# Kernel tuning notes

Measured on AMD Instinct MI355X. Metric: run time of the kernel, lower is better.

The kernel has to match this reference:

```python
import jax, jax.numpy as jnp
import numpy as np

N = 8  # block_size

def _dct_matrix(n):
    m = np.zeros((n, n), dtype=np.float32)
    for k in range(n):
        for t in range(n):
            if k == 0:
                m[k, t] = np.sqrt(1.0 / n)
            else:
                m[k, t] = np.sqrt(2.0 / n) * np.cos(np.pi * k * (2 * t + 1) / (2 * n))
    return m

def _zigzag(n):
    idxs = np.zeros((n, n), dtype=np.int64)
    idx = 0
    for s in range(2 * n - 1):
        if s % 2 == 0:
            rng = range(min(s, n - 1), max(0, s - n + 1) - 1, -1)
        else:
            rng = range(max(0, s - n + 1), min(s, n - 1) + 1)
        for i in rng:
            j = s - i
            if 0 <= i < n and 0 <= j < n:
                idxs[i, j] = idx
                idx += 1
    return idxs

def _band_masks(n):
    zz = _zigzag(n)
    total = n * n
    lo_t, hi_t = total // 3, 2 * total // 3
    low = (zz < lo_t).astype(np.float32)
    mid = ((zz >= lo_t) & (zz < hi_t)).astype(np.float32)
    high = (zz >= hi_t).astype(np.float32)
    return low, mid, high

_D = jnp.asarray(_dct_matrix(N))
_LOW, _MID, _HIGH = (jnp.asarray(m) for m in _band_masks(N))

def setup_inputs() -> dict:
    key = jax.random.key(0)
    x = jax.random.normal(key, (16, 3, 512, 512), dtype=jnp.float32)
    band_scale = jnp.ones((3,), dtype=jnp.float32)
    return {"x": x, "band_scale": band_scale}

def reference(x, band_scale):
    B, C, H, W = x.shape
    pad_h = (N - H % N) % N
    pad_w = (N - W % N) % N
    if pad_h > 0 or pad_w > 0:
        x = jnp.pad(x, ((0, 0), (0, 0), (0, pad_h), (0, pad_w)), mode="reflect")
    Hp, Wp = x.shape[2], x.shape[3]
    nH, nW = Hp // N, Wp // N
    # [B,C,nH,N,nW,N] -> blocks [B,C,nH,nW,N,N]
    blocks = x.reshape(B, C, nH, N, nW, N).transpose(0, 1, 2, 4, 3, 5)
    # 2D DCT-II: D @ X @ D^T
    coeffs = jnp.einsum("km,bchwmn,ln->bchwkl", _D, blocks, _D)

    def idct_band(mask, scale):
        c = coeffs * mask
        # IDCT: D^T @ C @ D
        sp = jnp.einsum("km,bchwkl,ln->bchwmn", _D, c, _D)
        out = sp.transpose(0, 1, 2, 4, 3, 5).reshape(B, C, Hp, Wp)
        return out[:, :, :H, :W] * scale

    low = idct_band(_LOW, band_scale[0])
    mid = idct_band(_MID, band_scale[1])
    high = idct_band(_HIGH, band_scale[2])
    return (low, mid, high)
```

## Files before the change

### kernel.cpp

```cpp
#include <hip/hip_runtime.h>

#define IMG   512
#define NIMG  48
#define PLANE (IMG * IMG)
#define OUTCH ((size_t)NIMG * PLANE)
#define NTHREADS (NIMG * 64 * 64)

__device__ constexpr float Dm[8][8] = {
  { 0.3535533905932738f, 0.3535533905932738f, 0.3535533905932738f, 0.3535533905932738f,
    0.3535533905932738f, 0.3535533905932738f, 0.3535533905932738f, 0.3535533905932738f},
  { 0.4903926402016152f, 0.4157348061512726f, 0.2777851165098011f, 0.0975451610080642f,
   -0.0975451610080642f,-0.2777851165098011f,-0.4157348061512726f,-0.4903926402016152f},
  { 0.4619397662556434f, 0.1913417161825449f,-0.1913417161825449f,-0.4619397662556434f,
   -0.4619397662556434f,-0.1913417161825449f, 0.1913417161825449f, 0.4619397662556434f},
  { 0.4157348061512726f,-0.0975451610080642f,-0.4903926402016152f,-0.2777851165098011f,
    0.2777851165098011f, 0.4903926402016152f, 0.0975451610080642f,-0.4157348061512726f},
  { 0.3535533905932738f,-0.3535533905932738f,-0.3535533905932738f, 0.3535533905932738f,
    0.3535533905932738f,-0.3535533905932738f,-0.3535533905932738f, 0.3535533905932738f},
  { 0.2777851165098011f,-0.4903926402016152f, 0.0975451610080642f, 0.4157348061512726f,
   -0.4157348061512726f,-0.0975451610080642f, 0.4903926402016152f,-0.2777851165098011f},
  { 0.1913417161825449f,-0.4619397662556434f, 0.4619397662556434f,-0.1913417161825449f,
   -0.1913417161825449f, 0.4619397662556434f,-0.4619397662556434f, 0.1913417161825449f},
  { 0.0975451610080642f,-0.2777851165098011f, 0.4157348061512726f,-0.4903926402016152f,
    0.4903926402016152f,-0.4157348061512726f, 0.2777851165098011f,-0.0975451610080642f},
};

__device__ constexpr int ZZ[8][8] = {
  {  0,  1,  5,  6, 14, 15, 27, 28},
  {  2,  4,  7, 13, 16, 26, 29, 42},
  {  3,  8, 12, 17, 25, 30, 41, 43},
  {  9, 11, 18, 24, 31, 40, 44, 53},
  { 10, 19, 23, 32, 39, 45, 52, 54},
  { 20, 22, 33, 38, 46, 51, 55, 60},
  { 21, 34, 37, 47, 50, 56, 59, 61},
  { 35, 36, 48, 49, 57, 58, 62, 63},
};

template <int LO, int HI>
__device__ __forceinline__ void idct_band_store(const float A[8][8],
                                                float* __restrict__ dst,
                                                float scale) {
  float U[8][8];
#pragma unroll
  for (int l = 0; l < 8; ++l) {
#pragma unroll
    for (int m = 0; m < 8; ++m) {
      float acc = 0.0f;
#pragma unroll
      for (int k = 0; k < 8; ++k) {
        if (ZZ[k][l] >= LO && ZZ[k][l] < HI) acc += Dm[k][m] * A[k][l];
      }
      U[m][l] = acc;
    }
  }
#pragma unroll
  for (int m = 0; m < 8; ++m) {
    float t[8];
#pragma unroll
    for (int n = 0; n < 8; ++n) {
      float acc = 0.0f;
#pragma unroll
      for (int l = 0; l < 8; ++l) acc += U[m][l] * Dm[l][n];
      t[n] = acc * scale;
    }
    *(float4*)(dst + (size_t)m * IMG)     = make_float4(t[0], t[1], t[2], t[3]);
    *(float4*)(dst + (size_t)m * IMG + 4) = make_float4(t[4], t[5], t[6], t[7]);
  }
}

__global__ __launch_bounds__(256) void dct_decomp_kernel(
    const float* __restrict__ x, const float* __restrict__ band_scale,
    float* __restrict__ out) {
  int tid = blockIdx.x * 256 + threadIdx.x;
  if (tid >= NTHREADS) return;

  int bw  = tid & 63;
  int bh  = (tid >> 6) & 63;
  int img = tid >> 12;

  size_t base = ((size_t)img * IMG + (size_t)bh * 8) * IMG + (size_t)bw * 8;
  const float* src = x + base;

  float A[8][8];
#pragma unroll
  for (int r = 0; r < 8; ++r) {
    float4 v0 = *(const float4*)(src + (size_t)r * IMG);
    float4 v1 = *(const float4*)(src + (size_t)r * IMG + 4);
    A[r][0] = v0.x; A[r][1] = v0.y; A[r][2] = v0.z; A[r][3] = v0.w;
    A[r][4] = v1.x; A[r][5] = v1.y; A[r][6] = v1.z; A[r][7] = v1.w;
  }

#pragma unroll
  for (int m = 0; m < 8; ++m) {
    float t[8];
#pragma unroll
    for (int l = 0; l < 8; ++l) {
      float acc = 0.0f;
#pragma unroll
      for (int n = 0; n < 8; ++n) acc += A[m][n] * Dm[l][n];
      t[l] = acc;
    }
#pragma unroll
    for (int l = 0; l < 8; ++l) A[m][l] = t[l];
  }
#pragma unroll
  for (int l = 0; l < 8; ++l) {
    float t[8];
#pragma unroll
    for (int k = 0; k < 8; ++k) {
      float acc = 0.0f;
#pragma unroll
      for (int m = 0; m < 8; ++m) acc += Dm[k][m] * A[m][l];
      t[k] = acc;
    }
#pragma unroll
    for (int k = 0; k < 8; ++k) A[k][l] = t[k];
  }

  float s0 = band_scale[0];
  float s1 = band_scale[1];
  float s2 = band_scale[2];

  idct_band_store< 0, 21>(A, out + base,             s0);
  idct_band_store<21, 42>(A, out + OUTCH + base,     s1);
  idct_band_store<42, 64>(A, out + 2 * OUTCH + base, s2);
}

extern "C" void kernel_launch(void* const* d_in, const int* in_sizes, int n_in,
                              void* d_out, int out_size, void* d_ws, size_t ws_size,
                              hipStream_t stream) {
  const float* x          = (const float*)d_in[0];
  const float* band_scale = (const float*)d_in[1];
  float* out              = (float*)d_out;

  dim3 grid(NTHREADS / 256);
  dim3 block(256);
  dct_decomp_kernel<<<grid, block, 0, stream>>>(x, band_scale, out);
}
```

Before: 190.8 us.

## Split each 8x8 DCT block across eight threads and derive high band as residual

Work moves from one thread per 8x8 block to eight threads per block, one row each. Row and column passes exchange data through a small per-group LDS tile instead of holding a full 64-element block in registers. Band masks become per-row bitmasks, and the high band is computed as the input minus the low and mid reconstructions instead of a third inverse DCT. This cuts register pressure and raises occupancy, and it makes the global accesses finer-grained. In exchange it relies on wave-lockstep ordering of the LDS accesses with no barrier, and the residual form adds small floating-point differences.

```diff
diff --git a/kernel.cpp b/kernel.cpp
--- a/kernel.cpp
+++ b/kernel.cpp
@@ -2,9 +2,9 @@
 
 #define IMG   512
 #define NIMG  48
-#define PLANE (IMG * IMG)
-#define OUTCH ((size_t)NIMG * PLANE)
-#define NTHREADS (NIMG * 64 * 64)
+#define NBLK  (NIMG * 64 * 64)
+#define OUTCH ((size_t)NIMG * IMG * IMG)
+#define NTHREADS (NBLK * 8)
 
 __device__ constexpr float Dm[8][8] = {
   { 0.3535533905932738f, 0.3535533905932738f, 0.3535533905932738f, 0.3535533905932738f,
@@ -25,105 +25,112 @@
     0.4903926402016152f,-0.4157348061512726f, 0.2777851165098011f,-0.0975451610080642f},
 };
 
-__device__ constexpr int ZZ[8][8] = {
-  {  0,  1,  5,  6, 14, 15, 27, 28},
-  {  2,  4,  7, 13, 16, 26, 29, 42},
-  {  3,  8, 12, 17, 25, 30, 41, 43},
-  {  9, 11, 18, 24, 31, 40, 44, 53},
-  { 10, 19, 23, 32, 39, 45, 52, 54},
-  { 20, 22, 33, 38, 46, 51, 55, 60},
-  { 21, 34, 37, 47, 50, 56, 59, 61},
-  { 35, 36, 48, 49, 57, 58, 62, 63},
-};
+#define LO_BITS64  0x00000103070F1F3FULL
+#define MID_BITS64 0x01070E1C3870E0C0ULL
 
-template <int LO, int HI>
-__device__ __forceinline__ void idct_band_store(const float A[8][8],
-                                                float* __restrict__ dst,
-                                                float scale) {
-  float U[8][8];
+__global__ __launch_bounds__(256, 4) void dct_decomp_kernel(
+    const float* __restrict__ x, const float* __restrict__ band_scale,
+    float* __restrict__ out) {
+  __shared__ float lds[32 * 72];
+
+  const int tx = threadIdx.x;
+  const int r  = tx & 7;
+  const int gq = tx >> 3;
+  const int g  = (blockIdx.x << 5) | gq;
+
+  const int bw  = g & 63;
+  const int bh  = (g >> 6) & 63;
+  const int img = g >> 12;
+
+  const size_t base = ((size_t)img * IMG + (size_t)bh * 8) * IMG + (size_t)bw * 8;
+  const float* src = x + base + (size_t)r * IMG;
+
+  float xr[8];
+  {
+    float4 v0 = *(const float4*)(src);
+    float4 v1 = *(const float4*)(src + 4);
+    xr[0]=v0.x; xr[1]=v0.y; xr[2]=v0.z; xr[3]=v0.w;
+    xr[4]=v1.x; xr[5]=v1.y; xr[6]=v1.z; xr[7]=v1.w;
+  }
+
+  float t[8];
 #pragma unroll
   for (int l = 0; l < 8; ++l) {
+    float acc = 0.0f;
+#pragma unroll
+    for (int n = 0; n < 8; ++n) acc += xr[n] * Dm[l][n];
+    t[l] = acc;
+  }
+
+  float* L = lds + gq * 72;
+
+#pragma unroll
+  for (int l = 0; l < 8; ++l) L[l * 8 + r] = t[l];
+  float tc[8];
+#pragma unroll
+  for (int m = 0; m < 8; ++m) tc[m] = L[r * 8 + m];
+
+  float c[8];
+#pragma unroll
+  for (int k = 0; k < 8; ++k) {
+    float acc = 0.0f;
+#pragma unroll
+    for (int m = 0; m < 8; ++m) acc += Dm[k][m] * tc[m];
+    c[k] = acc;
+  }
+
+  const unsigned lo_m  = (unsigned)(LO_BITS64  >> (r * 8)) & 0xFFu;
+  const unsigned mid_m = (unsigned)(MID_BITS64 >> (r * 8)) & 0xFFu;
+
+  auto band_sp = [&](unsigned mbits, float sp[8]) {
+    float cm[8];
+#pragma unroll
+    for (int k = 0; k < 8; ++k) cm[k] = (mbits & (1u << k)) ? c[k] : 0.0f;
+    float u[8];
 #pragma unroll
     for (int m = 0; m < 8; ++m) {
       float acc = 0.0f;
 #pragma unroll
-      for (int k = 0; k < 8; ++k) {
-        if (ZZ[k][l] >= LO && ZZ[k][l] < HI) acc += Dm[k][m] * A[k][l];
-      }
-      U[m][l] = acc;
+      for (int k = 0; k < 8; ++k) acc += Dm[k][m] * cm[k];
+      u[m] = acc;
     }
-  }
 #pragma unroll
-  for (int m = 0; m < 8; ++m) {
-    float t[8];
+    for (int m = 0; m < 8; ++m) L[m * 8 + r] = u[m];
+    float ur[8];
+#pragma unroll
+    for (int l = 0; l < 8; ++l) ur[l] = L[r * 8 + l];
 #pragma unroll
     for (int n = 0; n < 8; ++n) {
       float acc = 0.0f;
 #pragma unroll
-      for (int l = 0; l < 8; ++l) acc += U[m][l] * Dm[l][n];
-      t[n] = acc * scale;
+      for (int l = 0; l < 8; ++l) acc += ur[l] * Dm[l][n];
+      sp[n] = acc;
     }
-    *(float4*)(dst + (size_t)m * IMG)     = make_float4(t[0], t[1], t[2], t[3]);
-    *(float4*)(dst + (size_t)m * IMG + 4) = make_float4(t[4], t[5], t[6], t[7]);
-  }
-}
+  };
 
-__global__ __launch_bounds__(256) void dct_decomp_kernel(
-    const float* __restrict__ x, const float* __restrict__ band_scale,
-    float* __restrict__ out) {
-  int tid = blockIdx.x * 256 + threadIdx.x;
-  if (tid >= NTHREADS) return;
+  float splo[8], spmid[8];
+  band_sp(lo_m,  splo);
+  band_sp(mid_m, spmid);
 
-  int bw  = tid & 63;
-  int bh  = (tid >> 6) & 63;
-  int img = tid >> 12;
+  const float s0 = band_scale[0];
+  const float s1 = band_scale[1];
+  const float s2 = band_scale[2];
 
-  size_t base = ((size_t)img * IMG + (size_t)bh * 8) * IMG + (size_t)bw * 8;
-  const float* src = x + base;
+  float* dst0 = out + base + (size_t)r * IMG;
+  float* dst1 = dst0 + OUTCH;
+  float* dst2 = dst1 + OUTCH;
 
-  float A[8][8];
+  *(float4*)(dst0)     = make_float4(splo[0]*s0, splo[1]*s0, splo[2]*s0, splo[3]*s0);
+  *(float4*)(dst0 + 4) = make_float4(splo[4]*s0, splo[5]*s0, splo[6]*s0, splo[7]*s0);
+
+  *(float4*)(dst1)     = make_float4(spmid[0]*s1, spmid[1]*s1, spmid[2]*s1, spmid[3]*s1);
+  *(float4*)(dst1 + 4) = make_float4(spmid[4]*s1, spmid[5]*s1, spmid[6]*s1, spmid[7]*s1);
+
+  float h[8];
 #pragma unroll
-  for (int r = 0; r < 8; ++r) {
-    float4 v0 = *(const float4*)(src + (size_t)r * IMG);
-    float4 v1 = *(const float4*)(src + (size_t)r * IMG + 4);
-    A[r][0] = v0.x; A[r][1] = v0.y; A[r][2] = v0.z; A[r][3] = v0.w;
-    A[r][4] = v1.x; A[r][5] = v1.y; A[r][6] = v1.z; A[r][7] = v1.w;
-  }
-
-#pragma unroll
-  for (int m = 0; m < 8; ++m) {
-    float t[8];
-#pragma unroll
-    for (int l = 0; l < 8; ++l) {
-      float acc = 0.0f;
-#pragma unroll
-      for (int n = 0; n < 8; ++n) acc += A[m][n] * Dm[l][n];
-      t[l] = acc;
-    }
-#pragma unroll
-    for (int l = 0; l < 8; ++l) A[m][l] = t[l];
-  }
-#pragma unroll
-  for (int l = 0; l < 8; ++l) {
-    float t[8];
-#pragma unroll
-    for (int k = 0; k < 8; ++k) {
-      float acc = 0.0f;
-#pragma unroll
-      for (int m = 0; m < 8; ++m) acc += Dm[k][m] * A[m][l];
-      t[k] = acc;
-    }
-#pragma unroll
-    for (int k = 0; k < 8; ++k) A[k][l] = t[k];
-  }
-
-  float s0 = band_scale[0];
-  float s1 = band_scale[1];
-  float s2 = band_scale[2];
-
-  idct_band_store< 0, 21>(A, out + base,             s0);
-  idct_band_store<21, 42>(A, out + OUTCH + base,     s1);
-  idct_band_store<42, 64>(A, out + 2 * OUTCH + base, s2);
+  for (int n = 0; n < 8; ++n) h[n] = (xr[n] - splo[n] - spmid[n]) * s2;
+  *(float4*)(dst2)     = make_float4(h[0], h[1], h[2], h[3]);
+  *(float4*)(dst2 + 4) = make_float4(h[4], h[5], h[6], h[7]);
 }
 
 extern "C" void kernel_launch(void* const* d_in, const int* in_sizes, int n_in,
```

Measured after the change: 191.1 us. About the same (+0.2%).
